# Kernel tuning notes

Hardware: AMD Instinct MI355X
Metric: run time of the kernel (lower is better)

The kernel has to match this reference:

```python
import jax, jax.numpy as jnp
import numpy as np

N = 100000      # nodes
E = 3200000     # edges (avg degree 32)
NODE, EDGE, H = 11, 2, 32
EPS = 1e-5


def setup_inputs() -> dict:
    key = jax.random.key(0)
    ks = jax.random.split(key, 12)
    def w(k, shape):  # small init like torch Linear
        return jax.random.normal(k, shape, dtype=jnp.float32) * 0.1
    inp = {
        'x': jax.random.normal(ks[0], (N, NODE), dtype=jnp.float32),
        'edge_attr': jax.random.normal(ks[1], (E, EDGE), dtype=jnp.float32),
        'edge_index': jax.random.randint(ks[2], (2, E), 0, N),
        # mlp1: Lin(13,32)-BN-ReLU-Lin(32,32)-BN-ReLU
        'w1a': w(ks[3], (NODE + EDGE, H)), 'b1a': jnp.zeros(H), 'g1a': jnp.ones(H), 'be1a': jnp.zeros(H),
        'w1b': w(ks[4], (H, H)),           'b1b': jnp.zeros(H), 'g1b': jnp.ones(H), 'be1b': jnp.zeros(H),
        # mlp2: Lin(43,32)-BN-ReLU then Lin(32,1)-ReLU (no BN on last)
        'w2a': w(ks[5], (NODE + H, H)), 'b2a': jnp.zeros(H), 'g2a': jnp.ones(H), 'be2a': jnp.zeros(H),
        'w2b': w(ks[6], (H, 1)),        'b2b': jnp.zeros(1),
        # power: Lin(11,32)-BN-ReLU-Lin(32,1)-BN-ReLU
        'wpa': w(ks[7], (NODE, H)), 'bpa': jnp.zeros(H), 'gpa': jnp.ones(H), 'bepa': jnp.zeros(H),
        'wpb': w(ks[8], (H, 1)),    'bpb': jnp.zeros(1), 'gpb': jnp.ones(1), 'bepb': jnp.zeros(1),
    }
    return inp


def _bn(x, g, b):
    # training-mode BatchNorm1d (batch stats, biased variance), like torch default
    mu = x.mean(0, keepdims=True)
    var = ((x - mu) ** 2).mean(0, keepdims=True)
    return (x - mu) * jax.lax.rsqrt(var + EPS) * g + b


def _conv(x, edge_index, edge_attr,
          w1a, b1a, g1a, be1a, w1b, b1b, g1b, be1b,
          w2a, b2a, g2a, be2a, w2b, b2b):
    src, dst = edge_index[0], edge_index[1]
    # message: cat([x_j, edge_attr]) -> mlp1
    m = jnp.concatenate([x[src], edge_attr], axis=1)          # [E, 13]
    m = jax.nn.relu(_bn(m @ w1a + b1a, g1a, be1a))            # [E, 32]
    m = jax.nn.relu(_bn(m @ w1b + b1b, g1b, be1b))            # [E, 32]
    # aggr='max' scatter to destination nodes
    agg = jax.ops.segment_max(m, dst, num_segments=x.shape[0])
    agg = jnp.where(jnp.isneginf(agg), 0.0, agg)              # empty segments -> 0
    # update: cat([x, aggr_out]) -> mlp2, then replace last feature column
    h = jax.nn.relu(_bn(jnp.concatenate([x, agg], axis=1) @ w2a + b2a, g2a, be2a))
    comb = jax.nn.relu(h @ w2b + b2b)                         # [N, 1]
    return jnp.concatenate([x[:, :-1], comb], axis=1)         # [N, 11]


def reference(x, edge_attr, edge_index,
              w1a, b1a, g1a, be1a, w1b, b1b, g1b, be1b,
              w2a, b2a, g2a, be2a, w2b, b2b,
              wpa, bpa, gpa, bepa, wpb, bpb, gpb, bepb):
    for _ in range(3):
        x = _conv(x, edge_index, edge_attr,
                  w1a, b1a, g1a, be1a, w1b, b1b, g1b, be1b,
                  w2a, b2a, g2a, be2a, w2b, b2b)
    h = jax.nn.relu(_bn(x @ wpa + bpa, gpa, bepa))
    out = jax.nn.relu(_bn(h @ wpb + bpb, gpb, bepb))
    return out
```

## Files before the change

kernel.cpp:

```cpp
#include <hip/hip_runtime.h>
#include <hip/hip_bf16.h>
#include <cstddef>

#define NN 100000
#define EE 3200000
#define NBIN 64
static const float EF = 3200000.0f;
#define INVN (1.0f / 100000.0f)


__device__ __forceinline__ float wsum(float v) {
  #pragma unroll
  for (int off = 32; off > 0; off >>= 1) v += __shfl_down(v, off, 64);
  return v;
}

__device__ __forceinline__ void reduce64(float sum[32], float ssq[32], float* red,
                                         float* __restrict__ gsum, float* __restrict__ gssq) {
  const int wid = threadIdx.x >> 6, lane = threadIdx.x & 63;
  #pragma unroll
  for (int j = 0; j < 32; j++) {
    float a = wsum(sum[j]);
    float b = wsum(ssq[j]);
    if (lane == 0) { red[wid * 64 + j] = a; red[wid * 64 + 32 + j] = b; }
  }
  __syncthreads();
  if (threadIdx.x < 64) {
    float t = red[threadIdx.x] + red[64 + threadIdx.x] + red[128 + threadIdx.x] + red[192 + threadIdx.x];
    if (threadIdx.x < 32) unsafeAtomicAdd(&gsum[threadIdx.x], t);
    else                  unsafeAtomicAdd(&gssq[threadIdx.x - 32], t);
  }
}

__device__ __forceinline__ void loadrow(const float* __restrict__ xp, int s, float in[13]) {
  const float4* xr = reinterpret_cast<const float4*>(xp + (size_t)s * 12);
  float4 r0 = xr[0], r1 = xr[1], r2 = xr[2];
  in[0]=r0.x; in[1]=r0.y; in[2]=r0.z; in[3]=r0.w; in[4]=r1.x; in[5]=r1.y; in[6]=r1.z; in[7]=r1.w;
  in[8]=r2.x; in[9]=r2.y; in[10]=r2.z;
}

__device__ __forceinline__ unsigned long long packsea(float x, float y) {
  unsigned int xq = (unsigned int)(fmaf(x, 16384.f, 131072.f) + 0.5f);
  unsigned int yq = (unsigned int)(fmaf(y, 16384.f, 131072.f) + 0.5f);
  return (1ULL << 54) | ((unsigned long long)yq << 27) | (unsigned long long)xq;
}


__global__ __launch_bounds__(256) void k_wprep(const float* __restrict__ w1b,
    const float* __restrict__ b1b, const float* __restrict__ g1b,
    const float* __restrict__ w2a, const float* __restrict__ b2a,
    const float* __restrict__ wpa, const float* __restrict__ bpa,
    float* __restrict__ w2tf, float* __restrict__ b1bf,
    float* __restrict__ w2aT, float* __restrict__ wpaT) {
  int t = threadIdx.x;
  for (int i = t; i < 1024; i += 256) {
    int j = i >> 5, k = i & 31;
    float d = (g1b[j] >= 0.f) ? 1.f : -1.f;
    w2tf[j * 32 + k] = d * w1b[k * 32 + j];
  }
  for (int i = t; i < 32 * 43; i += 256) { int j = i & 31, k = i >> 5; w2aT[j * 44 + k] = w2a[k * 32 + j]; }
  for (int i = t; i < 32 * 11; i += 256) { int j = i & 31, k = i >> 5; wpaT[j * 12 + k] = wpa[k * 32 + j]; }
  if (t < 32) {
    float d = (g1b[t] >= 0.f) ? 1.f : -1.f;
    b1bf[t] = d * b1b[t];
    w2aT[t * 44 + 43] = b2a[t];
    wpaT[t * 12 + 11] = bpa[t];
  }
}

__global__ __launch_bounds__(256) void k_prep(const int* __restrict__ dst, const int* __restrict__ src,
    const float* __restrict__ ea, int* __restrict__ cnt, int* __restrict__ rank,
    unsigned long long* __restrict__ nsd, float* __restrict__ cmom) {
  float p0 = 0, p1 = 0, p2 = 0, p3 = 0, p4 = 0;
  const int S = gridDim.x * 256;
  for (int g = blockIdx.x * 256 + threadIdx.x; g < EE / 4; g += S) {
    int4 d4 = reinterpret_cast<const int4*>(dst)[g];
    int4 s4 = reinterpret_cast<const int4*>(src)[g];
    float4 e0 = reinterpret_cast<const float4*>(ea)[2 * g];
    float4 e1 = reinterpret_cast<const float4*>(ea)[2 * g + 1];
    int r0 = atomicAdd(&cnt[d4.x], 1);
    int r1 = atomicAdd(&cnt[d4.y], 1);
    int r2 = atomicAdd(&cnt[d4.z], 1);
    int r3 = atomicAdd(&cnt[d4.w], 1);
    reinterpret_cast<int4*>(rank)[g] = make_int4(r0, r1, r2, r3);
    atomicAdd(&nsd[s4.x], packsea(e0.x, e0.y));
    atomicAdd(&nsd[s4.y], packsea(e0.z, e0.w));
    atomicAdd(&nsd[s4.z], packsea(e1.x, e1.y));
    atomicAdd(&nsd[s4.w], packsea(e1.z, e1.w));
    p0 += e0.x * e0.x + e0.z * e0.z + e1.x * e1.x + e1.z * e1.z;
    p1 += e0.x * e0.y + e0.z * e0.w + e1.x * e1.y + e1.z * e1.w;
    p2 += e0.y * e0.y + e0.w * e0.w + e1.y * e1.y + e1.w * e1.w;
    p3 += e0.x + e0.z + e1.x + e1.z;
    p4 += e0.y + e0.w + e1.y + e1.w;
  }
  p0 = wsum(p0); p1 = wsum(p1); p2 = wsum(p2); p3 = wsum(p3); p4 = wsum(p4);
  if ((threadIdx.x & 63) == 0) {
    unsafeAtomicAdd(&cmom[0], p0); unsafeAtomicAdd(&cmom[1], p1); unsafeAtomicAdd(&cmom[2], p2);
    unsafeAtomicAdd(&cmom[3], p3); unsafeAtomicAdd(&cmom[4], p4);
  }
}

__global__ __launch_bounds__(1024) void k_scan(const int* __restrict__ cnt,
                                               int* __restrict__ starts) {
  __shared__ int part[1024];
  const int T = 1024, CH = (NN + T - 1) / T;
  int t = threadIdx.x;
  int lo = t * CH, hi = min(lo + CH, NN);
  int s = 0;
  for (int i = lo; i < hi; i++) s += cnt[i];
  part[t] = s; __syncthreads();
  for (int off = 1; off < T; off <<= 1) {
    int v = (t >= off) ? part[t - off] : 0;
    __syncthreads();
    part[t] += v;
    __syncthreads();
  }
  int run = part[t] - s;
  for (int i = lo; i < hi; i++) { starts[i] = run; run += cnt[i]; }
  if (t == T - 1) starts[NN] = EE;
}

__global__ __launch_bounds__(256) void k_scatter(const int* __restrict__ dst, const int* __restrict__ src,
    const float* __restrict__ ea, const int* __restrict__ starts, const int* __restrict__ rank,
    int4* __restrict__ edg) {
  const int S = gridDim.x * 256;
  for (int g = blockIdx.x * 256 + threadIdx.x; g < EE / 4; g += S) {
    int4 d4 = reinterpret_cast<const int4*>(dst)[g];
    int4 s4 = reinterpret_cast<const int4*>(src)[g];
    int4 r4 = reinterpret_cast<const int4*>(rank)[g];
    float4 e0 = reinterpret_cast<const float4*>(ea)[2 * g];
    float4 e1 = reinterpret_cast<const float4*>(ea)[2 * g + 1];
    edg[starts[d4.x] + r4.x] = make_int4(s4.x, __float_as_int(e0.x), __float_as_int(e0.y), 0);
    edg[starts[d4.y] + r4.y] = make_int4(s4.y, __float_as_int(e0.z), __float_as_int(e0.w), 0);
    edg[starts[d4.z] + r4.z] = make_int4(s4.z, __float_as_int(e1.x), __float_as_int(e1.y), 0);
    edg[starts[d4.w] + r4.w] = make_int4(s4.w, __float_as_int(e1.z), __float_as_int(e1.w), 0);
  }
}

__global__ __launch_bounds__(256) void k_xp(const float* __restrict__ x, float* __restrict__ xp) {
  int n = blockIdx.x * 256 + threadIdx.x;
  if (n >= NN) return;
  float v[11];
  #pragma unroll
  for (int k = 0; k < 11; k++) v[k] = x[(size_t)n * 11 + k];
  float4* o = reinterpret_cast<float4*>(xp + (size_t)n * 12);
  o[0] = make_float4(v[0], v[1], v[2], v[3]);
  o[1] = make_float4(v[4], v[5], v[6], v[7]);
  o[2] = make_float4(v[8], v[9], v[10], 0.f);
}

__global__ __launch_bounds__(256) void k_mom(const float* __restrict__ xp,
                                             const unsigned long long* __restrict__ nsd,
                                             float* __restrict__ mom) {
  const int n = blockIdx.x * 256 + threadIdx.x;
  const int lane = threadIdx.x & 63;
  float v[11]; float w = 0.f; float sx = 0.f, sy = 0.f;
  #pragma unroll
  for (int k = 0; k < 11; k++) v[k] = 0.f;
  if (n < NN) {
    unsigned long long pv = nsd[n];
    float dg = (float)(unsigned int)(pv >> 54);
    float sxf = (float)(unsigned int)(pv & 0x7FFFFFFull);
    float syf = (float)(unsigned int)((pv >> 27) & 0x7FFFFFFull);
    w = dg;
    sx = sxf * (1.f / 16384.f) - 8.f * dg;
    sy = syf * (1.f / 16384.f) - 8.f * dg;
    loadrow(xp, n, v);
  }
  int ch = 0;
  #pragma unroll
  for (int a = 0; a < 11; a++) {
    float r = wsum(w * v[a]);
    if (lane == 0) unsafeAtomicAdd(&mom[ch], r);
    ch++;
  }
  #pragma unroll
  for (int a = 0; a < 11; a++) {
    #pragma unroll
    for (int b = a; b < 11; b++) {
      float r = wsum(w * v[a] * v[b]);
      if (lane == 0) unsafeAtomicAdd(&mom[ch], r);
      ch++;
    }
  }
  #pragma unroll
  for (int a = 0; a < 11; a++) {
    float rx = wsum(v[a] * sx);
    if (lane == 0) unsafeAtomicAdd(&mom[ch], rx);
    ch++;
    float ry = wsum(v[a] * sy);
    if (lane == 0) unsafeAtomicAdd(&mom[ch], ry);
    ch++;
  }
}

__device__ __forceinline__ float msym(const float* mom, const float* cmom, int k, int l) {
  int a = min(k, l), b = max(k, l);
  if (b < 11) return mom[11 + a * 11 - a * (a - 1) / 2 + (b - a)];
  if (a < 11) return mom[77 + a * 2 + (b - 11)];
  return cmom[(a - 11) + (b - 11)];
}

__global__ __launch_bounds__(256) void k_P(const float* __restrict__ xp,
    const float* __restrict__ mom, const float* __restrict__ cmom,
    const float* __restrict__ w1a, const float* __restrict__ b1a,
    const float* __restrict__ g1a, const float* __restrict__ be1a,
    float* __restrict__ wexy, float* __restrict__ statsbase, float* __restrict__ P) {
  __shared__ float w1fs[32 * 14];
  const int t = threadIdx.x;
  if (t < 32) {
    const int jj = t;
    float w[13], S[13];
    #pragma unroll
    for (int k = 0; k < 13; k++) w[k] = w1a[k * 32 + jj];
    #pragma unroll
    for (int k = 0; k < 11; k++) S[k] = mom[k];
    S[11] = cmom[3]; S[12] = cmom[4];
    float lin = 0.f;
    #pragma unroll
    for (int k = 0; k < 13; k++) lin = fmaf(w[k], S[k], lin);
    float quad = 0.f;
    #pragma unroll
    for (int k = 0; k < 13; k++)
      #pragma unroll
      for (int l = 0; l < 13; l++) quad = fmaf(w[k] * w[l], msym(mom, cmom, k, l), quad);
    const float invE = 1.f / EF;
    float b = b1a[jj];
    float mean = fmaf(lin, invE, b);
    float ey2 = (quad + 2.f * b * lin) * invE + b * b;
    float var = fmaxf(ey2 - mean * mean, 0.f);
    float A = g1a[jj] * rsqrtf(var + 1e-5f);
    float C = be1a[jj] - mean * A;
    #pragma unroll
    for (int k = 0; k < 11; k++) w1fs[jj * 14 + k] = A * w[k];
    w1fs[jj * 14 + 11] = 0.f; w1fs[jj * 14 + 12] = 0.f;
    w1fs[jj * 14 + 13] = fmaf(A, b, C);
    if (blockIdx.x == 0) { wexy[jj] = A * w[11]; wexy[32 + jj] = A * w[12]; }
  }
  if (blockIdx.x == 0 && t >= 64 && t < 128) statsbase[t] = 0.f;
  __syncthreads();
  const int n = blockIdx.x * 256 + t;
  if (n >= NN) return;
  float xv[11];
  loadrow(xp, n, xv);
  float4* op = reinterpret_cast<float4*>(P + (size_t)n * 32);
  #pragma unroll
  for (int jj = 0; jj < 8; jj++) {
    float o[4];
    #pragma unroll
    for (int u = 0; u < 4; u++) {
      int j = 4 * jj + u;
      const float* wr = w1fs + j * 14;
      float acc = wr[13];
      #pragma unroll
      for (int k = 0; k < 11; k++) acc = fmaf(xv[k], wr[k], acc);
      o[u] = acc;
    }
    op[jj] = make_float4(o[0], o[1], o[2], o[3]);
  }
}

__global__ __launch_bounds__(256, 6) void k_fusedagg(
    const int* __restrict__ starts, const int4* __restrict__ edg,
    const float* __restrict__ P, const float* __restrict__ wexy,
    const float* __restrict__ w2tf, const float* __restrict__ b1bf,
    float* __restrict__ tzb, float* __restrict__ gms, float* __restrict__ gzq) {
  __shared__ float smx[4][2][32];
  __shared__ float redm[4][32], redq[4][32];
  const int tid = threadIdx.x;
  const int wid = tid >> 6, lane = tid & 63;
  const int half = lane >> 5, l = lane & 31;
  const int c0 = l & 15, h = (l >> 4) & 1;
  const int n = blockIdx.x * 8 + wid * 2 + half;
  const float wex = wexy[l], wey = wexy[32 + l], bz = b1bf[l];
  const float4* wcA = reinterpret_cast<const float4*>(w2tf + (size_t)c0 * 32 + 16 * h);
  const float4* wcB = reinterpret_cast<const float4*>(w2tf + (size_t)(c0 + 16) * 32 + 16 * h);
  const float4 a0 = wcA[0], a1 = wcA[1], a2 = wcA[2], a3 = wcA[3];
  const float4 b0 = wcB[0], b1 = wcB[1], b2 = wcB[2], b3 = wcB[3];
  float tz = -3.0e38f, zq = 0.f, ms = 0.f;
  int lo = 0, hi = 0;
  if (n < NN) { lo = starts[n]; hi = starts[n + 1]; }
  float* msl = &smx[wid][half][0];
  const float* mrd = msl + 16 * h;
  int sl = lo;
  int4 eA = make_int4(0, 0, 0, 0), eB = make_int4(0, 0, 0, 0);
  float pA = 0.f;
  if (sl < hi) {
    eA = edg[sl];
    pA = P[(size_t)eA.x * 32 + l];
  }
  if (sl + 1 < hi) eB = edg[sl + 1];
  while (sl < hi) {
    int4 eC = eB;
    if (sl + 2 < hi) eC = edg[sl + 2];
    float pN = pA;
    if (sl + 1 < hi) pN = P[(size_t)eB.x * 32 + l];
    const float ex = __int_as_float(eA.y), ey = __int_as_float(eA.z);
    const float m = fmaxf(0.f, fmaf(ex, wex, fmaf(ey, wey, pA)));
    ms += m;
    msl[l] = m;
    __builtin_amdgcn_wave_barrier();
    const float4 m0 = *reinterpret_cast<const float4*>(mrd + 0);
    const float4 m1 = *reinterpret_cast<const float4*>(mrd + 4);
    const float4 m2 = *reinterpret_cast<const float4*>(mrd + 8);
    const float4 m3 = *reinterpret_cast<const float4*>(mrd + 12);
    __builtin_amdgcn_wave_barrier();
    float zA0 = 0.f, zA1 = 0.f, zB0 = 0.f, zB1 = 0.f;
    zA0 = fmaf(m0.x, a0.x, zA0); zA1 = fmaf(m0.y, a0.y, zA1);
    zA0 = fmaf(m0.z, a0.z, zA0); zA1 = fmaf(m0.w, a0.w, zA1);
    zA0 = fmaf(m1.x, a1.x, zA0); zA1 = fmaf(m1.y, a1.y, zA1);
    zA0 = fmaf(m1.z, a1.z, zA0); zA1 = fmaf(m1.w, a1.w, zA1);
    zA0 = fmaf(m2.x, a2.x, zA0); zA1 = fmaf(m2.y, a2.y, zA1);
    zA0 = fmaf(m2.z, a2.z, zA0); zA1 = fmaf(m2.w, a2.w, zA1);
    zA0 = fmaf(m3.x, a3.x, zA0); zA1 = fmaf(m3.y, a3.y, zA1);
    zA0 = fmaf(m3.z, a3.z, zA0); zA1 = fmaf(m3.w, a3.w, zA1);
    zB0 = fmaf(m0.x, b0.x, zB0); zB1 = fmaf(m0.y, b0.y, zB1);
    zB0 = fmaf(m0.z, b0.z, zB0); zB1 = fmaf(m0.w, b0.w, zB1);
    zB0 = fmaf(m1.x, b1.x, zB0); zB1 = fmaf(m1.y, b1.y, zB1);
    zB0 = fmaf(m1.z, b1.z, zB0); zB1 = fmaf(m1.w, b1.w, zB1);
    zB0 = fmaf(m2.x, b2.x, zB0); zB1 = fmaf(m2.y, b2.y, zB1);
    zB0 = fmaf(m2.z, b2.z, zB0); zB1 = fmaf(m2.w, b2.w, zB1);
    zB0 = fmaf(m3.x, b3.x, zB0); zB1 = fmaf(m3.y, b3.y, zB1);
    zB0 = fmaf(m3.z, b3.z, zB0); zB1 = fmaf(m3.w, b3.w, zB1);
    float pAh = zA0 + zA1;
    float pBh = zB0 + zB1;
    pAh += __shfl_xor(pAh, 16, 64);
    pBh += __shfl_xor(pBh, 16, 64);
    const float z = ((l & 16) ? pBh : pAh) + bz;
    tz = fmaxf(tz, z);
    zq = fmaf(z, z, zq);
    eA = eB; eB = eC; pA = pN;
    ++sl;
  }
  if (n < NN) tzb[(size_t)n * 32 + l] = tz;
  float msT = ms + __shfl_xor(ms, 32, 64);
  float zqT = zq + __shfl_xor(zq, 32, 64);
  if (lane < 32) { redm[wid][l] = msT; redq[wid][l] = zqT; }
  __syncthreads();
  if (tid < 32) {
    float a = redm[0][tid] + redm[1][tid] + redm[2][tid] + redm[3][tid];
    float b = redq[0][tid] + redq[1][tid] + redq[2][tid] + redq[3][tid];
    const int bin = blockIdx.x & (NBIN - 1);
    unsafeAtomicAdd(&gms[bin * 32 + tid], a);
    unsafeAtomicAdd(&gzq[bin * 32 + tid], b);
  }
}

__global__ __launch_bounds__(256) void k_hpre2(const float* __restrict__ xp,
    const float* __restrict__ tzb, const int* __restrict__ starts,
    const float* __restrict__ gms, const float* __restrict__ gzq,
    const float* __restrict__ w1b, const float* __restrict__ b1b,
    const float* __restrict__ g1b, const float* __restrict__ be1b,
    const float* __restrict__ w2aT,
    float* __restrict__ hpre, float* __restrict__ gsum, float* __restrict__ gssq) {
  __shared__ float red[256], a2s[32], c2s[32], smm[32], szq[32];
  const int t = threadIdx.x;
  if (t < 32) {
    float msj = 0.f, zqj = 0.f;
    for (int b = 0; b < NBIN; b++) { msj += gms[b * 32 + t]; zqj += gzq[b * 32 + t]; }
    smm[t] = msj; szq[t] = zqj;
  }
  __syncthreads();
  if (t < 32) {
    float zs = EF * b1b[t];
    #pragma unroll
    for (int k = 0; k < 32; k++) zs = fmaf(w1b[k * 32 + t], smm[k], zs);
    const float invE = 1.f / EF;
    float mu = zs * invE;
    float var = fmaxf(szq[t] * invE - mu * mu, 0.f);
    float A = g1b[t] * rsqrtf(var + 1e-5f);
    float C = be1b[t] - mu * A;
    float d = (g1b[t] >= 0.f) ? 1.f : -1.f;
    a2s[t] = A * d; c2s[t] = C;
  }
  __syncthreads();
  const int n = blockIdx.x * 256 + t;
  float hh[32], hv[32];
  #pragma unroll
  for (int j = 0; j < 32; j++) hv[j] = 0.f;
  if (n < NN) {
    float xv[11];
    loadrow(xp, n, xv);
    const int dg = starts[n + 1] - starts[n];
    float av[32];
    if (dg > 0) {
      const float4* tp = reinterpret_cast<const float4*>(tzb + (size_t)n * 32);
      #pragma unroll
      for (int j = 0; j < 8; j++) {
        float4 v = tp[j];
        av[4 * j]     = fmaxf(0.f, fmaf(a2s[4 * j],     v.x, c2s[4 * j]));
        av[4 * j + 1] = fmaxf(0.f, fmaf(a2s[4 * j + 1], v.y, c2s[4 * j + 1]));
        av[4 * j + 2] = fmaxf(0.f, fmaf(a2s[4 * j + 2], v.z, c2s[4 * j + 2]));
        av[4 * j + 3] = fmaxf(0.f, fmaf(a2s[4 * j + 3], v.w, c2s[4 * j + 3]));
      }
    } else {
      #pragma unroll
      for (int j = 0; j < 32; j++) av[j] = 0.f;
    }
    #pragma unroll
    for (int j = 0; j < 32; j++) {
      const float* wr = w2aT + j * 44;
      float acc = wr[43];
      #pragma unroll
      for (int k = 0; k < 11; k++) acc = fmaf(xv[k], wr[k], acc);
      #pragma unroll
      for (int k = 0; k < 32; k++) acc = fmaf(av[k], wr[11 + k], acc);
      hv[j] = acc;
    }
    float4* hp = reinterpret_cast<float4*>(hpre + (size_t)n * 32);
    #pragma unroll
    for (int j = 0; j < 8; j++)
      hp[j] = make_float4(hv[4 * j], hv[4 * j + 1], hv[4 * j + 2], hv[4 * j + 3]);
  }
  #pragma unroll
  for (int j = 0; j < 32; j++) hh[j] = hv[j] * hv[j];
  reduce64(hv, hh, red, gsum, gssq);
}

__global__ __launch_bounds__(256) void k_comb(const float* __restrict__ hpre,
    const float* __restrict__ SUM3, const float* __restrict__ SSQ3,
    const float* __restrict__ g2a, const float* __restrict__ be2a,
    const float* __restrict__ w2b, const float* __restrict__ b2b, float* __restrict__ xp,
    float* __restrict__ mom, float* __restrict__ gms, float* __restrict__ gzq) {
  __shared__ float a3s[32], c3s[32];
  const int t = threadIdx.x;
  if (t < 32) {
    float mu = SUM3[t] * INVN;
    float var = fmaxf(SSQ3[t] * INVN - mu * mu, 0.f);
    float s = rsqrtf(var + 1e-5f) * g2a[t];
    a3s[t] = s; c3s[t] = be2a[t] - mu * s;
  }
  __syncthreads();
  const int n = blockIdx.x * 256 + t;
  if (n < NN) {
    const float4* hp = reinterpret_cast<const float4*>(hpre + (size_t)n * 32);
    float acc = b2b[0];
    #pragma unroll
    for (int j = 0; j < 8; j++) {
      float4 v = hp[j];
      acc += fmaxf(0.f, fmaf(v.x, a3s[4 * j],     c3s[4 * j]))     * w2b[4 * j];
      acc += fmaxf(0.f, fmaf(v.y, a3s[4 * j + 1], c3s[4 * j + 1])) * w2b[4 * j + 1];
      acc += fmaxf(0.f, fmaf(v.z, a3s[4 * j + 2], c3s[4 * j + 2])) * w2b[4 * j + 2];
      acc += fmaxf(0.f, fmaf(v.w, a3s[4 * j + 3], c3s[4 * j + 3])) * w2b[4 * j + 3];
    }
    xp[(size_t)n * 12 + 10] = fmaxf(acc, 0.f);
  }
  if (blockIdx.x == 0) {
    if (t < 128) mom[t] = 0.f;
    for (int i = t; i < NBIN * 32; i += 256) { gms[i] = 0.f; gzq[i] = 0.f; }
  }
}


__global__ __launch_bounds__(256) void k_p5(const float* __restrict__ xp, const float* __restrict__ wpaT,
                                            float* __restrict__ ybuf,
                                            float* __restrict__ gsum, float* __restrict__ gssq) {
  __shared__ float red[256];
  const int n = blockIdx.x * 256 + threadIdx.x;
  float y[32], yy[32];
  #pragma unroll
  for (int j = 0; j < 32; j++) y[j] = 0.f;
  if (n < NN) {
    float xv[11];
    loadrow(xp, n, xv);
    #pragma unroll
    for (int j = 0; j < 32; j++) {
      const float* wr = wpaT + j * 12;
      float acc = wr[11];
      #pragma unroll
      for (int k = 0; k < 11; k++) acc = fmaf(xv[k], wr[k], acc);
      y[j] = acc;
    }
    float4* yp = reinterpret_cast<float4*>(ybuf + (size_t)n * 32);
    #pragma unroll
    for (int j = 0; j < 8; j++)
      yp[j] = make_float4(y[4 * j], y[4 * j + 1], y[4 * j + 2], y[4 * j + 3]);
  }
  #pragma unroll
  for (int j = 0; j < 32; j++) yy[j] = y[j] * y[j];
  reduce64(y, yy, red, gsum, gssq);
}

__global__ __launch_bounds__(256) void k_p6(const float* __restrict__ ybuf,
    const float* __restrict__ SUM4, const float* __restrict__ SSQ4,
    const float* __restrict__ gpa, const float* __restrict__ bepa,
    const float* __restrict__ wpb, const float* __restrict__ bpb,
    float* __restrict__ yq, float* __restrict__ gsum, float* __restrict__ gssq) {
  __shared__ float red[8], a4s[32], c4s[32];
  const int t = threadIdx.x;
  if (t < 32) {
    float mu = SUM4[t] * INVN;
    float var = fmaxf(SSQ4[t] * INVN - mu * mu, 0.f);
    float s = rsqrtf(var + 1e-5f) * gpa[t];
    a4s[t] = s; c4s[t] = bepa[t] - mu * s;
  }
  __syncthreads();
  const int n = blockIdx.x * 256 + t;
  float sum = 0.f, ssq = 0.f;
  if (n < NN) {
    const float4* yp = reinterpret_cast<const float4*>(ybuf + (size_t)n * 32);
    float q = bpb[0];
    #pragma unroll
    for (int j = 0; j < 8; j++) {
      float4 v = yp[j];
      q = fmaf(fmaxf(0.f, fmaf(v.x, a4s[4 * j],     c4s[4 * j])),     wpb[4 * j],     q);
      q = fmaf(fmaxf(0.f, fmaf(v.y, a4s[4 * j + 1], c4s[4 * j + 1])), wpb[4 * j + 1], q);
      q = fmaf(fmaxf(0.f, fmaf(v.z, a4s[4 * j + 2], c4s[4 * j + 2])), wpb[4 * j + 2], q);
      q = fmaf(fmaxf(0.f, fmaf(v.w, a4s[4 * j + 3], c4s[4 * j + 3])), wpb[4 * j + 3], q);
    }
    yq[n] = q;
    sum = q; ssq = q * q;
  }
  float s = wsum(sum), qq = wsum(ssq);
  const int wid = t >> 6, lane = t & 63;
  if (lane == 0) { red[wid] = s; red[4 + wid] = qq; }
  __syncthreads();
  if (t == 0) {
    unsafeAtomicAdd(&gsum[0], red[0] + red[1] + red[2] + red[3]);
    unsafeAtomicAdd(&gssq[0], red[4] + red[5] + red[6] + red[7]);
  }
}

__global__ __launch_bounds__(256) void k_p7(const float* __restrict__ yq,
    const float* __restrict__ SUM5, const float* __restrict__ SSQ5,
    const float* __restrict__ gpb, const float* __restrict__ bepb, float* __restrict__ out) {
  const int n = blockIdx.x * 256 + threadIdx.x;
  if (n >= NN) return;
  float mu = SUM5[0] * INVN;
  float var = fmaxf(SSQ5[0] * INVN - mu * mu, 0.f);
  float a5 = rsqrtf(var + 1e-5f) * gpb[0];
  float c5 = bepb[0] - mu * a5;
  out[n] = fmaxf(0.f, fmaf(yq[n], a5, c5));
}


extern "C" void kernel_launch(void* const* d_in, const int* in_sizes, int n_in,
                              void* d_out, int out_size, void* d_ws, size_t ws_size,
                              hipStream_t stream) {
  const float* x    = (const float*)d_in[0];
  const float* ea   = (const float*)d_in[1];
  const int*   ei   = (const int*)d_in[2];
  const int*   srcp = ei;
  const int*   dstp = ei + EE;
  const float* w1a = (const float*)d_in[3],  *b1a = (const float*)d_in[4];
  const float* g1a = (const float*)d_in[5],  *be1a = (const float*)d_in[6];
  const float* w1b = (const float*)d_in[7],  *b1b = (const float*)d_in[8];
  const float* g1b = (const float*)d_in[9],  *be1b = (const float*)d_in[10];
  const float* w2a = (const float*)d_in[11], *b2a = (const float*)d_in[12];
  const float* g2a = (const float*)d_in[13], *be2a = (const float*)d_in[14];
  const float* w2b = (const float*)d_in[15], *b2b = (const float*)d_in[16];
  const float* wpa = (const float*)d_in[17], *bpa = (const float*)d_in[18];
  const float* gpa = (const float*)d_in[19], *bepa = (const float*)d_in[20];
  const float* wpb = (const float*)d_in[21], *bpb = (const float*)d_in[22];
  const float* gpb = (const float*)d_in[23], *bepb = (const float*)d_in[24];

  size_t off = 0;
  char* base = (char*)d_ws;
  auto alloc = [&](size_t bytes) -> void* {
    void* p = base + off;
    off += (bytes + 255) & ~(size_t)255;
    return p;
  };
  float* stats = (float*)alloc(2048);
  float* mom   = (float*)alloc(512);
  float* cmom  = (float*)alloc(256);
  float* gmsB  = (float*)alloc(NBIN * 32 * 4);
  float* gzqB  = (float*)alloc(NBIN * 32 * 4);
  float* wexy  = (float*)alloc(64 * 4);
  float* w2tf  = (float*)alloc(32 * 32 * 4);
  float* b1bf  = (float*)alloc(256);
  float* w2aT  = (float*)alloc(32 * 44 * 4);
  float* wpaT  = (float*)alloc(32 * 12 * 4);
  int*   cnt    = (int*)alloc(NN * 4);
  unsigned long long* nsd = (unsigned long long*)alloc((size_t)NN * 8);
  int*   starts = (int*)alloc((NN + 1) * 4);
  int*   rank   = (int*)alloc((size_t)EE * 4);
  int4*  edg    = (int4*)alloc((size_t)EE * 16);
  float* xp     = (float*)alloc((size_t)NN * 12 * 4);
  float* P      = (float*)alloc((size_t)NN * 32 * 4);
  float* tzb    = (float*)alloc((size_t)NN * 32 * 4);
  float* hpre   = (float*)alloc((size_t)NN * 32 * 4);
  float* yq     = (float*)alloc(NN * 4);

  float *SUM3 = stats + 64,  *SSQ3 = stats + 96;
  float *SUM4 = stats + 128, *SSQ4 = stats + 160;
  float *SUM5 = stats + 192, *SSQ5 = stats + 224;

  hipMemsetAsync(stats, 0, 2048, stream);
  hipMemsetAsync(mom, 0, 512 + 256, stream);
  hipMemsetAsync(gmsB, 0, NBIN * 32 * 4 * 2, stream);
  hipMemsetAsync(cnt, 0, NN * 4, stream);
  hipMemsetAsync(nsd, 0, (size_t)NN * 8, stream);

  const int GN = (NN + 255) / 256;
  const int GW = NN / 8;
  const int GE4 = (EE / 4 + 255) / 256;

  k_wprep  <<<1, 256, 0, stream>>>(w1b, b1b, g1b, w2a, b2a, wpa, bpa, w2tf, b1bf, w2aT, wpaT);
  k_prep   <<<GE4, 256, 0, stream>>>(dstp, srcp, ea, cnt, rank, nsd, cmom);
  k_scan   <<<1, 1024, 0, stream>>>(cnt, starts);
  k_scatter<<<GE4, 256, 0, stream>>>(dstp, srcp, ea, starts, rank, edg);
  k_xp     <<<GN, 256, 0, stream>>>(x, xp);

  for (int c = 0; c < 3; c++) {
    k_mom     <<<GN, 256, 0, stream>>>(xp, nsd, mom);
    k_P       <<<GN, 256, 0, stream>>>(xp, mom, cmom, w1a, b1a, g1a, be1a, wexy, stats, P);
    k_fusedagg<<<GW, 256, 0, stream>>>(starts, edg, P, wexy, w2tf, b1bf, tzb, gmsB, gzqB);
    k_hpre2   <<<GN, 256, 0, stream>>>(xp, tzb, starts, gmsB, gzqB, w1b, b1b, g1b, be1b,
                                       w2aT, hpre, SUM3, SSQ3);
    k_comb    <<<GN, 256, 0, stream>>>(hpre, SUM3, SSQ3, g2a, be2a, w2b, b2b, xp,
                                       mom, gmsB, gzqB);
  }

  k_p5<<<GN, 256, 0, stream>>>(xp, wpaT, hpre, SUM4, SSQ4);
  k_p6<<<GN, 256, 0, stream>>>(hpre, SUM4, SSQ4, gpa, bepa, wpb, bpb, yq, SUM5, SSQ5);
  k_p7<<<GN, 256, 0, stream>>>(yq, SUM5, SSQ5, gpb, bepb, (float*)d_out);
}
```

Before: 4.125 ms.

## Compute per-edge 32x32 matmul with bf16 split MFMA in persistent waves

Rewrites the fused edge-aggregation kernel so each wave handles one destination node and processes 32 edges at a time. The second MLP layer becomes a 32x32x16 bf16 MFMA, with hi/lo bf16 splitting (three products per K-half) to keep accuracy close to fp32. The old path did per-edge scalar FMAs with LDS exchanges. The grid becomes persistent (2048 blocks striding over nodes) with lower launch-bounds occupancy. This adds bf16 conversion overhead and wastes MFMA rows on low-degree tails, and the split precision only approximates fp32.

```diff
diff --git a/kernel.cpp b/kernel.cpp
--- a/kernel.cpp
+++ b/kernel.cpp
@@ -8,6 +8,9 @@
 static const float EF = 3200000.0f;
 #define INVN (1.0f / 100000.0f)
 
+typedef __attribute__((ext_vector_type(8))) short bf16x8;
+typedef __attribute__((ext_vector_type(16))) float f32x16;
+
 
 __device__ __forceinline__ float wsum(float v) {
   #pragma unroll
@@ -43,6 +46,16 @@
   unsigned int xq = (unsigned int)(fmaf(x, 16384.f, 131072.f) + 0.5f);
   unsigned int yq = (unsigned int)(fmaf(y, 16384.f, 131072.f) + 0.5f);
   return (1ULL << 54) | ((unsigned long long)yq << 27) | (unsigned long long)xq;
+}
+
+__device__ __forceinline__ short tobf(float f) {
+  return (short)((__float_as_uint(f) + 0x8000u) >> 16);
+}
+__device__ __forceinline__ float bfhi(float f) {
+  return __uint_as_float(__float_as_uint(f) & 0xFFFF0000u);
+}
+__device__ __forceinline__ short bfhi_s(float f) {
+  return (short)(__float_as_uint(f) >> 16);
 }
 
 
@@ -260,89 +273,121 @@
   }
 }
 
-__global__ __launch_bounds__(256, 6) void k_fusedagg(
+__global__ __launch_bounds__(256, 4) void k_fusedagg(
     const int* __restrict__ starts, const int4* __restrict__ edg,
     const float* __restrict__ P, const float* __restrict__ wexy,
     const float* __restrict__ w2tf, const float* __restrict__ b1bf,
     float* __restrict__ tzb, float* __restrict__ gms, float* __restrict__ gzq) {
-  __shared__ float smx[4][2][32];
-  __shared__ float redm[4][32], redq[4][32];
   const int tid = threadIdx.x;
   const int wid = tid >> 6, lane = tid & 63;
-  const int half = lane >> 5, l = lane & 31;
-  const int c0 = l & 15, h = (l >> 4) & 1;
-  const int n = blockIdx.x * 8 + wid * 2 + half;
-  const float wex = wexy[l], wey = wexy[32 + l], bz = b1bf[l];
-  const float4* wcA = reinterpret_cast<const float4*>(w2tf + (size_t)c0 * 32 + 16 * h);
-  const float4* wcB = reinterpret_cast<const float4*>(w2tf + (size_t)(c0 + 16) * 32 + 16 * h);
-  const float4 a0 = wcA[0], a1 = wcA[1], a2 = wcA[2], a3 = wcA[3];
-  const float4 b0 = wcB[0], b1 = wcB[1], b2 = wcB[2], b3 = wcB[3];
-  float tz = -3.0e38f, zq = 0.f, ms = 0.f;
-  int lo = 0, hi = 0;
-  if (n < NN) { lo = starts[n]; hi = starts[n + 1]; }
-  float* msl = &smx[wid][half][0];
-  const float* mrd = msl + 16 * h;
-  int sl = lo;
-  int4 eA = make_int4(0, 0, 0, 0), eB = make_int4(0, 0, 0, 0);
-  float pA = 0.f;
-  if (sl < hi) {
-    eA = edg[sl];
-    pA = P[(size_t)eA.x * 32 + l];
-  }
-  if (sl + 1 < hi) eB = edg[sl + 1];
-  while (sl < hi) {
-    int4 eC = eB;
-    if (sl + 2 < hi) eC = edg[sl + 2];
-    float pN = pA;
-    if (sl + 1 < hi) pN = P[(size_t)eB.x * 32 + l];
-    const float ex = __int_as_float(eA.y), ey = __int_as_float(eA.z);
-    const float m = fmaxf(0.f, fmaf(ex, wex, fmaf(ey, wey, pA)));
-    ms += m;
-    msl[l] = m;
-    __builtin_amdgcn_wave_barrier();
-    const float4 m0 = *reinterpret_cast<const float4*>(mrd + 0);
-    const float4 m1 = *reinterpret_cast<const float4*>(mrd + 4);
-    const float4 m2 = *reinterpret_cast<const float4*>(mrd + 8);
-    const float4 m3 = *reinterpret_cast<const float4*>(mrd + 12);
-    __builtin_amdgcn_wave_barrier();
-    float zA0 = 0.f, zA1 = 0.f, zB0 = 0.f, zB1 = 0.f;
-    zA0 = fmaf(m0.x, a0.x, zA0); zA1 = fmaf(m0.y, a0.y, zA1);
-    zA0 = fmaf(m0.z, a0.z, zA0); zA1 = fmaf(m0.w, a0.w, zA1);
-    zA0 = fmaf(m1.x, a1.x, zA0); zA1 = fmaf(m1.y, a1.y, zA1);
-    zA0 = fmaf(m1.z, a1.z, zA0); zA1 = fmaf(m1.w, a1.w, zA1);
-    zA0 = fmaf(m2.x, a2.x, zA0); zA1 = fmaf(m2.y, a2.y, zA1);
-    zA0 = fmaf(m2.z, a2.z, zA0); zA1 = fmaf(m2.w, a2.w, zA1);
-    zA0 = fmaf(m3.x, a3.x, zA0); zA1 = fmaf(m3.y, a3.y, zA1);
-    zA0 = fmaf(m3.z, a3.z, zA0); zA1 = fmaf(m3.w, a3.w, zA1);
-    zB0 = fmaf(m0.x, b0.x, zB0); zB1 = fmaf(m0.y, b0.y, zB1);
-    zB0 = fmaf(m0.z, b0.z, zB0); zB1 = fmaf(m0.w, b0.w, zB1);
-    zB0 = fmaf(m1.x, b1.x, zB0); zB1 = fmaf(m1.y, b1.y, zB1);
-    zB0 = fmaf(m1.z, b1.z, zB0); zB1 = fmaf(m1.w, b1.w, zB1);
-    zB0 = fmaf(m2.x, b2.x, zB0); zB1 = fmaf(m2.y, b2.y, zB1);
-    zB0 = fmaf(m2.z, b2.z, zB0); zB1 = fmaf(m2.w, b2.w, zB1);
-    zB0 = fmaf(m3.x, b3.x, zB0); zB1 = fmaf(m3.y, b3.y, zB1);
-    zB0 = fmaf(m3.z, b3.z, zB0); zB1 = fmaf(m3.w, b3.w, zB1);
-    float pAh = zA0 + zA1;
-    float pBh = zB0 + zB1;
-    pAh += __shfl_xor(pAh, 16, 64);
-    pBh += __shfl_xor(pBh, 16, 64);
-    const float z = ((l & 16) ? pBh : pAh) + bz;
-    tz = fmaxf(tz, z);
-    zq = fmaf(z, z, zq);
-    eA = eB; eB = eC; pA = pN;
-    ++sl;
-  }
-  if (n < NN) tzb[(size_t)n * 32 + l] = tz;
-  float msT = ms + __shfl_xor(ms, 32, 64);
+  const int j = lane & 31;
+  const int h = lane >> 5;
+  const int k1 = 8 * h;
+  const int k2 = 16 + 8 * h;
+  float wexk[16], weyk[16];
+  #pragma unroll
+  for (int i = 0; i < 8; i++) {
+    wexk[i]     = wexy[k1 + i];  weyk[i]     = wexy[32 + k1 + i];
+    wexk[8 + i] = wexy[k2 + i];  weyk[8 + i] = wexy[32 + k2 + i];
+  }
+  bf16x8 B1h, B1l, B2h, B2l;
+  #pragma unroll
+  for (int i = 0; i < 8; i++) {
+    float w1 = w2tf[j * 32 + k1 + i];
+    B1h[i] = bfhi_s(w1); B1l[i] = tobf(w1 - bfhi(w1));
+    float w2 = w2tf[j * 32 + k2 + i];
+    B2h[i] = bfhi_s(w2); B2l[i] = tobf(w2 - bfhi(w2));
+  }
+  const float bz = b1bf[j];
+  float ms[16];
+  #pragma unroll
+  for (int i = 0; i < 16; i++) ms[i] = 0.f;
+  float zq = 0.f;
+  const int nwaves = gridDim.x * 4;
+  for (int n = blockIdx.x * 4 + wid; n < NN; n += nwaves) {
+    const int lo = starts[n], hi = starts[n + 1];
+    float tzn = -3.0e38f;
+    for (int base = lo; base < hi; base += 32) {
+      const int v = min(hi - base, 32);
+      const bool ev = j < v;
+      const int4 r = edg[ev ? (base + j) : (hi - 1)];
+      const float ex = __int_as_float(r.y), ey = __int_as_float(r.z);
+      const float* pr = P + (size_t)r.x * 32;
+      const float4 p0 = *reinterpret_cast<const float4*>(pr + k1);
+      const float4 p1 = *reinterpret_cast<const float4*>(pr + k1 + 4);
+      const float4 p2 = *reinterpret_cast<const float4*>(pr + k2);
+      const float4 p3 = *reinterpret_cast<const float4*>(pr + k2 + 4);
+      const float vm = ev ? 1.f : 0.f;
+      float mv[16];
+      mv[0]  = vm * fmaxf(0.f, fmaf(ex, wexk[0],  fmaf(ey, weyk[0],  p0.x)));
+      mv[1]  = vm * fmaxf(0.f, fmaf(ex, wexk[1],  fmaf(ey, weyk[1],  p0.y)));
+      mv[2]  = vm * fmaxf(0.f, fmaf(ex, wexk[2],  fmaf(ey, weyk[2],  p0.z)));
+      mv[3]  = vm * fmaxf(0.f, fmaf(ex, wexk[3],  fmaf(ey, weyk[3],  p0.w)));
+      mv[4]  = vm * fmaxf(0.f, fmaf(ex, wexk[4],  fmaf(ey, weyk[4],  p1.x)));
+      mv[5]  = vm * fmaxf(0.f, fmaf(ex, wexk[5],  fmaf(ey, weyk[5],  p1.y)));
+      mv[6]  = vm * fmaxf(0.f, fmaf(ex, wexk[6],  fmaf(ey, weyk[6],  p1.z)));
+      mv[7]  = vm * fmaxf(0.f, fmaf(ex, wexk[7],  fmaf(ey, weyk[7],  p1.w)));
+      mv[8]  = vm * fmaxf(0.f, fmaf(ex, wexk[8],  fmaf(ey, weyk[8],  p2.x)));
+      mv[9]  = vm * fmaxf(0.f, fmaf(ex, wexk[9],  fmaf(ey, weyk[9],  p2.y)));
+      mv[10] = vm * fmaxf(0.f, fmaf(ex, wexk[10], fmaf(ey, weyk[10], p2.z)));
+      mv[11] = vm * fmaxf(0.f, fmaf(ex, wexk[11], fmaf(ey, weyk[11], p2.w)));
+      mv[12] = vm * fmaxf(0.f, fmaf(ex, wexk[12], fmaf(ey, weyk[12], p3.x)));
+      mv[13] = vm * fmaxf(0.f, fmaf(ex, wexk[13], fmaf(ey, weyk[13], p3.y)));
+      mv[14] = vm * fmaxf(0.f, fmaf(ex, wexk[14], fmaf(ey, weyk[14], p3.z)));
+      mv[15] = vm * fmaxf(0.f, fmaf(ex, wexk[15], fmaf(ey, weyk[15], p3.w)));
+      #pragma unroll
+      for (int i = 0; i < 16; i++) ms[i] += mv[i];
+      bf16x8 A1h, A1l, A2h, A2l;
+      #pragma unroll
+      for (int i = 0; i < 8; i++) {
+        A1h[i] = bfhi_s(mv[i]);     A1l[i] = tobf(mv[i] - bfhi(mv[i]));
+        A2h[i] = bfhi_s(mv[8 + i]); A2l[i] = tobf(mv[8 + i] - bfhi(mv[8 + i]));
+      }
+      f32x16 acc;
+      #pragma unroll
+      for (int i = 0; i < 16; i++) acc[i] = 0.f;
+      acc = __builtin_amdgcn_mfma_f32_32x32x16_bf16(A1h, B1h, acc, 0, 0, 0);
+      acc = __builtin_amdgcn_mfma_f32_32x32x16_bf16(A1h, B1l, acc, 0, 0, 0);
+      acc = __builtin_amdgcn_mfma_f32_32x32x16_bf16(A1l, B1h, acc, 0, 0, 0);
+      acc = __builtin_amdgcn_mfma_f32_32x32x16_bf16(A2h, B2h, acc, 0, 0, 0);
+      acc = __builtin_amdgcn_mfma_f32_32x32x16_bf16(A2h, B2l, acc, 0, 0, 0);
+      acc = __builtin_amdgcn_mfma_f32_32x32x16_bf16(A2l, B2h, acc, 0, 0, 0);
+      const int rb = base + 4 * h;
+      #pragma unroll
+      for (int rg = 0; rg < 16; rg++) {
+        const int row = (rg & 3) + 8 * (rg >> 2);
+        const bool rv = (rb + row) < hi;
+        const float z = acc[rg] + bz;
+        tzn = fmaxf(tzn, rv ? z : -3.0e38f);
+        const float zz = rv ? z : 0.f;
+        zq = fmaf(zz, zz, zq);
+      }
+    }
+    tzn = fmaxf(tzn, __shfl_xor(tzn, 32, 64));
+    if (lane < 32) tzb[(size_t)n * 32 + j] = tzn;
+  }
+  const int bin = blockIdx.x & (NBIN - 1);
   float zqT = zq + __shfl_xor(zq, 32, 64);
-  if (lane < 32) { redm[wid][l] = msT; redq[wid][l] = zqT; }
-  __syncthreads();
-  if (tid < 32) {
-    float a = redm[0][tid] + redm[1][tid] + redm[2][tid] + redm[3][tid];
-    float b = redq[0][tid] + redq[1][tid] + redq[2][tid] + redq[3][tid];
-    const int bin = blockIdx.x & (NBIN - 1);
-    unsafeAtomicAdd(&gms[bin * 32 + tid], a);
-    unsafeAtomicAdd(&gzq[bin * 32 + tid], b);
+  if (lane < 32) unsafeAtomicAdd(&gzq[bin * 32 + j], zqT);
+  #pragma unroll
+  for (int i = 0; i < 16; i++) {
+    ms[i] += __shfl_xor(ms[i], 16, 64);
+    ms[i] += __shfl_xor(ms[i], 8, 64);
+    ms[i] += __shfl_xor(ms[i], 4, 64);
+    ms[i] += __shfl_xor(ms[i], 2, 64);
+    ms[i] += __shfl_xor(ms[i], 1, 64);
+  }
+  if (lane == 0) {
+    #pragma unroll
+    for (int i = 0; i < 8; i++) unsafeAtomicAdd(&gms[bin * 32 + i], ms[i]);
+    #pragma unroll
+    for (int i = 0; i < 8; i++) unsafeAtomicAdd(&gms[bin * 32 + 16 + i], ms[8 + i]);
+  }
+  if (lane == 32) {
+    #pragma unroll
+    for (int i = 0; i < 8; i++) unsafeAtomicAdd(&gms[bin * 32 + 8 + i], ms[i]);
+    #pragma unroll
+    for (int i = 0; i < 8; i++) unsafeAtomicAdd(&gms[bin * 32 + 24 + i], ms[8 + i]);
   }
 }
 
@@ -593,7 +638,7 @@
   hipMemsetAsync(nsd, 0, (size_t)NN * 8, stream);
 
   const int GN = (NN + 255) / 256;
-  const int GW = NN / 8;
+  const int GW = 2048;
   const int GE4 = (EE / 4 + 255) / 256;
 
   k_wprep  <<<1, 256, 0, stream>>>(w1b, b1b, g1b, w2a, b2a, wpa, bpa, w2tf, b1bf, w2aT, wpaT);
```

Measured after the change: 3.831 ms. 1.08x faster.
